# Optimization experiments

Measured on AMD Instinct MI355X. Metric: run time of the kernel, lower is better.

Reference implementation:

```python
import jax, jax.numpy as jnp
import numpy as np

NUM_EXPERTS = 8
NUM_ROWS = 8192
HIDDEN = 2048
INTER = 2048
TOPK = 2


def setup_inputs() -> dict:
    key = jax.random.key(0)
    ks = jax.random.split(key, 5)
    x = jax.random.normal(ks[0], (NUM_ROWS, HIDDEN), dtype=jnp.float32)
    router_probs = jax.random.uniform(ks[1], (NUM_ROWS, NUM_EXPERTS), dtype=jnp.float32)
    # parameters ~ U(-0.1, 0.1) as in nn.init.uniform_
    fc1 = jax.random.uniform(ks[2], (NUM_EXPERTS, HIDDEN, INTER), minval=-0.1, maxval=0.1, dtype=jnp.float32)
    fc2 = jax.random.uniform(ks[3], (NUM_EXPERTS, INTER, HIDDEN), minval=-0.1, maxval=0.1, dtype=jnp.float32)
    fc3 = jax.random.uniform(ks[4], (NUM_EXPERTS, HIDDEN, INTER), minval=-0.1, maxval=0.1, dtype=jnp.float32)
    return {"x": x, "router_probs": router_probs, "fc1": fc1, "fc2": fc2, "fc3": fc3}


def reference(x, router_probs, fc1, fc2, fc3):
    # top-k routing + renormalize chosen probs
    topk_probs, topk_idx = jax.lax.top_k(router_probs, TOPK)  # [N, K]
    topk_probs = topk_probs / jnp.sum(topk_probs, axis=1, keepdims=True)
    # combine weight per (token, expert): scatter-add normalized probs
    n = x.shape[0]
    cw = jnp.zeros((n, NUM_EXPERTS), dtype=x.dtype)
    cw = cw.at[jnp.arange(n)[:, None], topk_idx].add(topk_probs)  # [N, E]
    # loop over fixed, small expert set (structurally distinct weights)
    out = jnp.zeros_like(x)
    for e in range(NUM_EXPERTS):
        h1 = x @ fc1[e]                      # [N, inter]
        h3 = x @ fc3[e]                      # [N, inter]
        act = jax.nn.silu(h1) * h3           # SwiGLU
        out = out + cw[:, e:e + 1] * (act @ fc2[e])
    return out
```

## Files before the change

kernel.cpp:

```cpp
#include <hip/hip_runtime.h>
#include <hip/hip_bf16.h>
#include <stdint.h>

#define NEXP 8
#define NROWS 8192
#define HID 2048
#define INTERN 2048
#define CAP 8192
#define KDIM 2048

typedef __attribute__((ext_vector_type(4))) float f32x4;
typedef __attribute__((ext_vector_type(8))) short bf16x8;

__device__ __forceinline__ unsigned short f2bf(float f) {
  union { float f; uint32_t u; } v; v.f = f;
  uint32_t u = v.u;
  uint32_t r = (u + 0x7fffu + ((u >> 16) & 1u)) >> 16;
  return (unsigned short)r;
}
__device__ __forceinline__ float bf2f(unsigned short u) {
  union { uint32_t u; float f; } v; v.u = (uint32_t)u << 16; return v.f;
}
__device__ __forceinline__ void gload16(const unsigned short* g, char* l) {
  __builtin_amdgcn_global_load_lds((const __attribute__((address_space(1))) void*)g,
                                   (__attribute__((address_space(3))) void*)l,
                                   16, 0, 0);
}

__global__ __launch_bounds__(256) void xcast_kernel(const float* __restrict__ x,
                                                    unsigned short* __restrict__ xb) {
  size_t i = ((size_t)blockIdx.x * 256 + threadIdx.x) * 8;
  size_t stride = (size_t)gridDim.x * 256 * 8;
  const size_t tot = (size_t)NROWS * HID;
  for (; i < tot; i += stride) {
    float4 a = *reinterpret_cast<const float4*>(x + i);
    float4 b = *reinterpret_cast<const float4*>(x + i + 4);
    unsigned short u[8];
    u[0] = f2bf(a.x); u[1] = f2bf(a.y); u[2] = f2bf(a.z); u[3] = f2bf(a.w);
    u[4] = f2bf(b.x); u[5] = f2bf(b.y); u[6] = f2bf(b.z); u[7] = f2bf(b.w);
    *reinterpret_cast<int4*>(xb + i) = *reinterpret_cast<const int4*>(u);
  }
}

__global__ void router_kernel(const float* __restrict__ probs,
                              int* __restrict__ cnt,
                              int* __restrict__ brow,
                              float* __restrict__ bw) {
  int row = blockIdx.x * blockDim.x + threadIdx.x;
  if (row >= NROWS) return;
  float p[8];
#pragma unroll
  for (int j = 0; j < 8; j++) p[j] = probs[row * 8 + j];
  int i1 = 0; float v1 = p[0];
#pragma unroll
  for (int j = 1; j < 8; j++) if (p[j] > v1) { v1 = p[j]; i1 = j; }
  int i2 = -1; float v2 = -1e30f;
#pragma unroll
  for (int j = 0; j < 8; j++) if (j != i1 && p[j] > v2) { v2 = p[j]; i2 = j; }
  float s = v1 + v2;
  float w1 = v1 / s, w2 = v2 / s;
  int pos1 = atomicAdd(&cnt[i1], 1);
  brow[i1 * CAP + pos1] = row; bw[i1 * CAP + pos1] = w1;
  int pos2 = atomicAdd(&cnt[i2], 1);
  brow[i2 * CAP + pos2] = row; bw[i2 * CAP + pos2] = w2;
}

__global__ void offsets_kernel(const int* __restrict__ cnt, int* __restrict__ ofs) {
  if (threadIdx.x == 0 && blockIdx.x == 0) {
    int a = 0;
    for (int e = 0; e < NEXP; e++) { ofs[e] = a; a += cnt[e]; }
  }
}

__global__ __launch_bounds__(256) void transpose_cast_kernel(const float* __restrict__ src,
                                                             unsigned short* __restrict__ dst) {
  __shared__ float tile[64][65];
  const int e = blockIdx.z;
  const int k0 = blockIdx.y * 64;
  const int n0 = blockIdx.x * 64;
  const float* s = src + (size_t)e * KDIM * KDIM;
  unsigned short* d = dst + (size_t)e * KDIM * KDIM;
  const int t = threadIdx.x;
  const int rr = t >> 4, cc = (t & 15) * 4;
#pragma unroll
  for (int i = 0; i < 4; i++) {
    float4 v = *reinterpret_cast<const float4*>(s + (size_t)(k0 + rr + i * 16) * KDIM + n0 + cc);
    tile[rr + i * 16][cc + 0] = v.x; tile[rr + i * 16][cc + 1] = v.y;
    tile[rr + i * 16][cc + 2] = v.z; tile[rr + i * 16][cc + 3] = v.w;
  }
  __syncthreads();
  const int n = t >> 2, kk0 = (t & 3) * 16;
  unsigned short u[16];
#pragma unroll
  for (int j = 0; j < 16; j++) u[j] = f2bf(tile[kk0 + j][n]);
  *reinterpret_cast<int4*>(d + (size_t)(n0 + n) * KDIM + k0 + kk0 + 0) = *reinterpret_cast<const int4*>(&u[0]);
  *reinterpret_cast<int4*>(d + (size_t)(n0 + n) * KDIM + k0 + kk0 + 8) = *reinterpret_cast<const int4*>(&u[8]);
}

template <int EPI>
__global__ __launch_bounds__(256, 2)
void gemm_kernel(const unsigned short* __restrict__ A,
                 const unsigned short* __restrict__ W,
                 const int* __restrict__ cnt, const int* __restrict__ ofs,
                 const int* __restrict__ brow, const float* __restrict__ bw,
                 unsigned short* __restrict__ hbuf,
                 float* __restrict__ out) {
  const int e = blockIdx.z, mt = blockIdx.y, nt = blockIdx.x;
  const int Me = cnt[e];
  if (mt * 128 >= Me) return;
  __shared__ unsigned short As[128 * 64];
  __shared__ unsigned short Bs[128 * 64];
  __shared__ int ridx[128];
  __shared__ float rww[128];
  const int t = threadIdx.x, lane = t & 63, wave = t >> 6;
  const int oe = ofs[e];
  if (t < 128) {
    int sl = mt * 128 + t;
    int ok = sl < Me;
    ridx[t] = ok ? brow[e * CAP + sl] : 0;
    rww[t] = ok ? bw[e * CAP + sl] : 0.f;
  }
  __syncthreads();

  const int srow = t >> 3;
  const int jslot = t & 7;
  const int kg = (jslot ^ (srow & 7)) * 8;
  const unsigned short *pA0, *pA1, *pA2, *pA3;
  if (EPI == 2) {
    int s;
    s = mt * 128 + srow +  0; if (s >= Me) s = 0; pA0 = A + (size_t)(oe + s) * KDIM + kg;
    s = mt * 128 + srow + 32; if (s >= Me) s = 0; pA1 = A + (size_t)(oe + s) * KDIM + kg;
    s = mt * 128 + srow + 64; if (s >= Me) s = 0; pA2 = A + (size_t)(oe + s) * KDIM + kg;
    s = mt * 128 + srow + 96; if (s >= Me) s = 0; pA3 = A + (size_t)(oe + s) * KDIM + kg;
  } else {
    pA0 = A + (size_t)ridx[srow +  0] * KDIM + kg;
    pA1 = A + (size_t)ridx[srow + 32] * KDIM + kg;
    pA2 = A + (size_t)ridx[srow + 64] * KDIM + kg;
    pA3 = A + (size_t)ridx[srow + 96] * KDIM + kg;
  }
  const unsigned short* Wb = W + (size_t)e * KDIM * KDIM;
  const unsigned short* pB0 = Wb + (size_t)(nt * 128 + srow +  0) * KDIM + kg;
  const unsigned short* pB1 = Wb + (size_t)(nt * 128 + srow + 32) * KDIM + kg;
  const unsigned short* pB2 = Wb + (size_t)(nt * 128 + srow + 64) * KDIM + kg;
  const unsigned short* pB3 = Wb + (size_t)(nt * 128 + srow + 96) * KDIM + kg;
  char* dA = (char*)As + wave * 1024;
  char* dB = (char*)Bs + wave * 1024;

  const int wm = wave >> 1, wn = wave & 1;
  const int l15 = lane & 15, kq = lane >> 4;
  const int c0 = (kq * 16) ^ ((l15 & 7) << 4);
  const int aoff = (wm * 64 + l15) * 128;
  const int boff = (wn * 64 + l15) * 128;

  f32x4 acc[4][4] = {};

  for (int k0 = 0; k0 < KDIM; k0 += 64) {
    gload16(pA0, dA);         gload16(pA1, dA + 4096);
    gload16(pA2, dA + 8192);  gload16(pA3, dA + 12288);
    gload16(pB0, dB);         gload16(pB1, dB + 4096);
    gload16(pB2, dB + 8192);  gload16(pB3, dB + 12288);
    pA0 += 64; pA1 += 64; pA2 += 64; pA3 += 64;
    pB0 += 64; pB1 += 64; pB2 += 64; pB3 += 64;
    __syncthreads();

    bf16x8 af0[4], bf0[4], af1[4], bf1[4];
#pragma unroll
    for (int i = 0; i < 4; i++) {
      af0[i] = *reinterpret_cast<const bf16x8*>((const char*)As + aoff + i * 2048 + c0);
      bf0[i] = *reinterpret_cast<const bf16x8*>((const char*)Bs + boff + i * 2048 + c0);
    }
#pragma unroll
    for (int mi = 0; mi < 4; mi++)
#pragma unroll
      for (int ni = 0; ni < 4; ni++)
        acc[mi][ni] = __builtin_amdgcn_mfma_f32_16x16x32_bf16(af0[mi], bf0[ni], acc[mi][ni], 0, 0, 0);
#pragma unroll
    for (int i = 0; i < 4; i++) {
      af1[i] = *reinterpret_cast<const bf16x8*>((const char*)As + aoff + i * 2048 + (c0 ^ 64));
      bf1[i] = *reinterpret_cast<const bf16x8*>((const char*)Bs + boff + i * 2048 + (c0 ^ 64));
    }
#pragma unroll
    for (int mi = 0; mi < 4; mi++)
#pragma unroll
      for (int ni = 0; ni < 4; ni++)
        acc[mi][ni] = __builtin_amdgcn_mfma_f32_16x16x32_bf16(af1[mi], bf1[ni], acc[mi][ni], 0, 0, 0);
    __syncthreads();
  }

  const int slot0 = oe + mt * 128;
#pragma unroll
  for (int mi = 0; mi < 4; mi++) {
#pragma unroll
    for (int ni = 0; ni < 4; ni++) {
      const int coln = nt * 128 + wn * 64 + ni * 16 + l15;
#pragma unroll
      for (int r = 0; r < 4; r++) {
        const int lrow = wm * 64 + mi * 16 + kq * 4 + r;
        if (mt * 128 + lrow < Me) {
          if (EPI == 0) {
            hbuf[(size_t)(slot0 + lrow) * KDIM + coln] = f2bf(acc[mi][ni][r]);
          } else if (EPI == 1) {
            size_t idx = (size_t)(slot0 + lrow) * KDIM + coln;
            float h1 = bf2f(hbuf[idx]);
            float sig = 1.f / (1.f + __expf(-h1));
            hbuf[idx] = f2bf(h1 * sig * acc[mi][ni][r]);
          } else {
            float v = acc[mi][ni][r] * rww[lrow];
            unsafeAtomicAdd(&out[(size_t)ridx[lrow] * HID + coln], v);
          }
        }
      }
    }
  }
}

extern "C" void kernel_launch(void* const* d_in, const int* in_sizes, int n_in,
                              void* d_out, int out_size, void* d_ws, size_t ws_size,
                              hipStream_t stream) {
  const float* x     = (const float*)d_in[0];
  const float* probs = (const float*)d_in[1];
  const float* fc1   = (const float*)d_in[2];
  const float* fc2   = (const float*)d_in[3];
  const float* fc3   = (const float*)d_in[4];
  float* out = (float*)d_out;

  char* ws = (char*)d_ws;
  const size_t WSZ = (size_t)NEXP * HID * INTERN * 2;
  unsigned short* wt1 = (unsigned short*)(ws);
  unsigned short* wt3 = (unsigned short*)(ws + WSZ);
  unsigned short* wt2 = (unsigned short*)(ws + 2 * WSZ);
  unsigned short* h1  = (unsigned short*)(ws + 3 * WSZ);
  unsigned short* xb  = (unsigned short*)(ws + 4 * WSZ);
  char* rbase = ws + 4 * WSZ + (size_t)NROWS * HID * 2;
  int*   brow = (int*)  (rbase);
  float* bw   = (float*)(rbase + (size_t)NEXP * CAP * 4);
  int*   cnt  = (int*)  (rbase + 2 * (size_t)NEXP * CAP * 4);
  int*   ofs  = (int*)  (rbase + 2 * (size_t)NEXP * CAP * 4 + 64);

  hipMemsetAsync(d_out, 0, (size_t)out_size * sizeof(float), stream);
  hipMemsetAsync(cnt, 0, 64, stream);

  xcast_kernel<<<2048, 256, 0, stream>>>(x, xb);
  transpose_cast_kernel<<<dim3(32, 32, 8), 256, 0, stream>>>(fc1, wt1);
  transpose_cast_kernel<<<dim3(32, 32, 8), 256, 0, stream>>>(fc3, wt3);
  transpose_cast_kernel<<<dim3(32, 32, 8), 256, 0, stream>>>(fc2, wt2);
  router_kernel<<<NROWS / 256, 256, 0, stream>>>(probs, cnt, brow, bw);
  offsets_kernel<<<1, 64, 0, stream>>>(cnt, ofs);

  gemm_kernel<0><<<dim3(INTERN / 128, CAP / 128, NEXP), 256, 0, stream>>>(xb, wt1, cnt, ofs, brow, bw, h1, out);
  gemm_kernel<1><<<dim3(INTERN / 128, CAP / 128, NEXP), 256, 0, stream>>>(xb, wt3, cnt, ofs, brow, bw, h1, out);
  gemm_kernel<2><<<dim3(HID / 128, CAP / 128, NEXP), 256, 0, stream>>>(h1, wt2, cnt, ofs, brow, bw, h1, out);
}
```

Before: 781.6 us.

## Fuse gate and up projection GEMMs into one dual-accumulator kernel

Merges the fc1 and fc3 expert GEMMs into one kernel that loads each gathered A tile once and computes both products into two accumulator sets, applying SiLU*up in the epilogue. This removes one pass over the gathered activations, the intermediate bf16 write and reread of h1, and one kernel launch. In exchange, register pressure doubles (two 4x4 f32x4 accumulators) under launch_bounds(256,2) and LDS use grows by a third tile, which may spill or cut occupancy. It also drops a rounding step, since h1 is no longer stored as bf16 before the activation.

```diff
diff --git a/kernel.cpp b/kernel.cpp
--- a/kernel.cpp
+++ b/kernel.cpp
@@ -97,14 +97,112 @@
   *reinterpret_cast<int4*>(d + (size_t)(n0 + n) * KDIM + k0 + kk0 + 8) = *reinterpret_cast<const int4*>(&u[8]);
 }
 
-template <int EPI>
 __global__ __launch_bounds__(256, 2)
-void gemm_kernel(const unsigned short* __restrict__ A,
-                 const unsigned short* __restrict__ W,
-                 const int* __restrict__ cnt, const int* __restrict__ ofs,
-                 const int* __restrict__ brow, const float* __restrict__ bw,
-                 unsigned short* __restrict__ hbuf,
-                 float* __restrict__ out) {
+void gemm13_kernel(const unsigned short* __restrict__ A,
+                   const unsigned short* __restrict__ W1,
+                   const unsigned short* __restrict__ W3,
+                   const int* __restrict__ cnt, const int* __restrict__ ofs,
+                   const int* __restrict__ brow,
+                   unsigned short* __restrict__ act) {
+  const int e = blockIdx.z, mt = blockIdx.y, nt = blockIdx.x;
+  const int Me = cnt[e];
+  if (mt * 128 >= Me) return;
+  __shared__ unsigned short As[128 * 64];
+  __shared__ unsigned short B1s[128 * 64];
+  __shared__ unsigned short B3s[128 * 64];
+  __shared__ int ridx[128];
+  const int t = threadIdx.x, lane = t & 63, wave = t >> 6;
+  const int oe = ofs[e];
+  if (t < 128) {
+    int sl = mt * 128 + t;
+    ridx[t] = (sl < Me) ? brow[e * CAP + sl] : 0;
+  }
+  __syncthreads();
+
+  const int srow = t >> 3;
+  const int kg = ((t & 7) ^ (srow & 7)) * 8;
+  const unsigned short* pA0 = A + (size_t)ridx[srow +  0] * KDIM + kg;
+  const unsigned short* pA1 = A + (size_t)ridx[srow + 32] * KDIM + kg;
+  const unsigned short* pA2 = A + (size_t)ridx[srow + 64] * KDIM + kg;
+  const unsigned short* pA3 = A + (size_t)ridx[srow + 96] * KDIM + kg;
+  const unsigned short* pB0 = W1 + (size_t)e * KDIM * KDIM + (size_t)(nt * 128 + srow) * KDIM + kg;
+  const ptrdiff_t dW = W3 - W1;
+  char* dA  = (char*)As  + wave * 1024;
+  char* dB1 = (char*)B1s + wave * 1024;
+  char* dB3 = (char*)B3s + wave * 1024;
+
+  const int wm = wave >> 1, wn = wave & 1;
+  const int l15 = lane & 15, kq = lane >> 4;
+  const int c0 = (kq * 16) ^ ((l15 & 7) << 4);
+  const int aoff = (wm * 64 + l15) * 128;
+  const int boff = (wn * 64 + l15) * 128;
+
+  f32x4 acc1[4][4] = {};
+  f32x4 acc3[4][4] = {};
+
+  for (int k0 = 0; k0 < KDIM; k0 += 64) {
+    gload16(pA0, dA);                    gload16(pA1, dA + 4096);
+    gload16(pA2, dA + 8192);             gload16(pA3, dA + 12288);
+    gload16(pB0,                dB1);    gload16(pB0 +  32 * KDIM, dB1 + 4096);
+    gload16(pB0 + 64 * KDIM,    dB1 + 8192); gload16(pB0 + 96 * KDIM, dB1 + 12288);
+    gload16(pB0 + dW,           dB3);    gload16(pB0 + dW + 32 * KDIM, dB3 + 4096);
+    gload16(pB0 + dW + 64 * KDIM, dB3 + 8192); gload16(pB0 + dW + 96 * KDIM, dB3 + 12288);
+    pA0 += 64; pA1 += 64; pA2 += 64; pA3 += 64; pB0 += 64;
+    __syncthreads();
+
+#pragma unroll
+    for (int h = 0; h < 2; h++) {
+      const int ch = h ? (c0 ^ 64) : c0;
+      bf16x8 af[4], bf[4];
+#pragma unroll
+      for (int i = 0; i < 4; i++)
+        af[i] = *reinterpret_cast<const bf16x8*>((const char*)As + aoff + i * 2048 + ch);
+#pragma unroll
+      for (int i = 0; i < 4; i++)
+        bf[i] = *reinterpret_cast<const bf16x8*>((const char*)B1s + boff + i * 2048 + ch);
+#pragma unroll
+      for (int mi = 0; mi < 4; mi++)
+#pragma unroll
+        for (int ni = 0; ni < 4; ni++)
+          acc1[mi][ni] = __builtin_amdgcn_mfma_f32_16x16x32_bf16(af[mi], bf[ni], acc1[mi][ni], 0, 0, 0);
+#pragma unroll
+      for (int i = 0; i < 4; i++)
+        bf[i] = *reinterpret_cast<const bf16x8*>((const char*)B3s + boff + i * 2048 + ch);
+#pragma unroll
+      for (int mi = 0; mi < 4; mi++)
+#pragma unroll
+        for (int ni = 0; ni < 4; ni++)
+          acc3[mi][ni] = __builtin_amdgcn_mfma_f32_16x16x32_bf16(af[mi], bf[ni], acc3[mi][ni], 0, 0, 0);
+    }
+    __syncthreads();
+  }
+
+  const int slot0 = oe + mt * 128;
+#pragma unroll
+  for (int mi = 0; mi < 4; mi++) {
+#pragma unroll
+    for (int ni = 0; ni < 4; ni++) {
+      const int coln = nt * 128 + wn * 64 + ni * 16 + l15;
+#pragma unroll
+      for (int r = 0; r < 4; r++) {
+        const int lrow = wm * 64 + mi * 16 + kq * 4 + r;
+        if (mt * 128 + lrow < Me) {
+          float h1 = acc1[mi][ni][r];
+          float h3 = acc3[mi][ni][r];
+          float sig = 1.f / (1.f + __expf(-h1));
+          act[(size_t)(slot0 + lrow) * KDIM + coln] = f2bf(h1 * sig * h3);
+        }
+      }
+    }
+  }
+}
+
+__global__ __launch_bounds__(256, 2)
+void gemm2_kernel(const unsigned short* __restrict__ A,
+                  const unsigned short* __restrict__ W,
+                  const int* __restrict__ cnt, const int* __restrict__ ofs,
+                  const int* __restrict__ brow, const float* __restrict__ bw,
+                  float* __restrict__ out) {
   const int e = blockIdx.z, mt = blockIdx.y, nt = blockIdx.x;
   const int Me = cnt[e];
   if (mt * 128 >= Me) return;
@@ -123,26 +221,14 @@
   __syncthreads();
 
   const int srow = t >> 3;
-  const int jslot = t & 7;
-  const int kg = (jslot ^ (srow & 7)) * 8;
+  const int kg = ((t & 7) ^ (srow & 7)) * 8;
+  int s;
   const unsigned short *pA0, *pA1, *pA2, *pA3;
-  if (EPI == 2) {
-    int s;
-    s = mt * 128 + srow +  0; if (s >= Me) s = 0; pA0 = A + (size_t)(oe + s) * KDIM + kg;
-    s = mt * 128 + srow + 32; if (s >= Me) s = 0; pA1 = A + (size_t)(oe + s) * KDIM + kg;
-    s = mt * 128 + srow + 64; if (s >= Me) s = 0; pA2 = A + (size_t)(oe + s) * KDIM + kg;
-    s = mt * 128 + srow + 96; if (s >= Me) s = 0; pA3 = A + (size_t)(oe + s) * KDIM + kg;
-  } else {
-    pA0 = A + (size_t)ridx[srow +  0] * KDIM + kg;
-    pA1 = A + (size_t)ridx[srow + 32] * KDIM + kg;
-    pA2 = A + (size_t)ridx[srow + 64] * KDIM + kg;
-    pA3 = A + (size_t)ridx[srow + 96] * KDIM + kg;
-  }
-  const unsigned short* Wb = W + (size_t)e * KDIM * KDIM;
-  const unsigned short* pB0 = Wb + (size_t)(nt * 128 + srow +  0) * KDIM + kg;
-  const unsigned short* pB1 = Wb + (size_t)(nt * 128 + srow + 32) * KDIM + kg;
-  const unsigned short* pB2 = Wb + (size_t)(nt * 128 + srow + 64) * KDIM + kg;
-  const unsigned short* pB3 = Wb + (size_t)(nt * 128 + srow + 96) * KDIM + kg;
+  s = mt * 128 + srow +  0; if (s >= Me) s = 0; pA0 = A + (size_t)(oe + s) * KDIM + kg;
+  s = mt * 128 + srow + 32; if (s >= Me) s = 0; pA1 = A + (size_t)(oe + s) * KDIM + kg;
+  s = mt * 128 + srow + 64; if (s >= Me) s = 0; pA2 = A + (size_t)(oe + s) * KDIM + kg;
+  s = mt * 128 + srow + 96; if (s >= Me) s = 0; pA3 = A + (size_t)(oe + s) * KDIM + kg;
+  const unsigned short* pB0 = W + (size_t)e * KDIM * KDIM + (size_t)(nt * 128 + srow) * KDIM + kg;
   char* dA = (char*)As + wave * 1024;
   char* dB = (char*)Bs + wave * 1024;
 
@@ -157,37 +243,29 @@
   for (int k0 = 0; k0 < KDIM; k0 += 64) {
     gload16(pA0, dA);         gload16(pA1, dA + 4096);
     gload16(pA2, dA + 8192);  gload16(pA3, dA + 12288);
-    gload16(pB0, dB);         gload16(pB1, dB + 4096);
-    gload16(pB2, dB + 8192);  gload16(pB3, dB + 12288);
-    pA0 += 64; pA1 += 64; pA2 += 64; pA3 += 64;
-    pB0 += 64; pB1 += 64; pB2 += 64; pB3 += 64;
+    gload16(pB0,             dB);        gload16(pB0 + 32 * KDIM, dB + 4096);
+    gload16(pB0 + 64 * KDIM, dB + 8192); gload16(pB0 + 96 * KDIM, dB + 12288);
+    pA0 += 64; pA1 += 64; pA2 += 64; pA3 += 64; pB0 += 64;
     __syncthreads();
 
-    bf16x8 af0[4], bf0[4], af1[4], bf1[4];
-#pragma unroll
-    for (int i = 0; i < 4; i++) {
-      af0[i] = *reinterpret_cast<const bf16x8*>((const char*)As + aoff + i * 2048 + c0);
-      bf0[i] = *reinterpret_cast<const bf16x8*>((const char*)Bs + boff + i * 2048 + c0);
+#pragma unroll
+    for (int h = 0; h < 2; h++) {
+      const int ch = h ? (c0 ^ 64) : c0;
+      bf16x8 af[4], bf[4];
+#pragma unroll
+      for (int i = 0; i < 4; i++) {
+        af[i] = *reinterpret_cast<const bf16x8*>((const char*)As + aoff + i * 2048 + ch);
+        bf[i] = *reinterpret_cast<const bf16x8*>((const char*)Bs + boff + i * 2048 + ch);
+      }
+#pragma unroll
+      for (int mi = 0; mi < 4; mi++)
+#pragma unroll
+        for (int ni = 0; ni < 4; ni++)
+          acc[mi][ni] = __builtin_amdgcn_mfma_f32_16x16x32_bf16(af[mi], bf[ni], acc[mi][ni], 0, 0, 0);
     }
-#pragma unroll
-    for (int mi = 0; mi < 4; mi++)
-#pragma unroll
-      for (int ni = 0; ni < 4; ni++)
-        acc[mi][ni] = __builtin_amdgcn_mfma_f32_16x16x32_bf16(af0[mi], bf0[ni], acc[mi][ni], 0, 0, 0);
-#pragma unroll
-    for (int i = 0; i < 4; i++) {
-      af1[i] = *reinterpret_cast<const bf16x8*>((const char*)As + aoff + i * 2048 + (c0 ^ 64));
-      bf1[i] = *reinterpret_cast<const bf16x8*>((const char*)Bs + boff + i * 2048 + (c0 ^ 64));
-    }
-#pragma unroll
-    for (int mi = 0; mi < 4; mi++)
-#pragma unroll
-      for (int ni = 0; ni < 4; ni++)
-        acc[mi][ni] = __builtin_amdgcn_mfma_f32_16x16x32_bf16(af1[mi], bf1[ni], acc[mi][ni], 0, 0, 0);
     __syncthreads();
   }
 
-  const int slot0 = oe + mt * 128;
 #pragma unroll
   for (int mi = 0; mi < 4; mi++) {
 #pragma unroll
@@ -197,17 +275,8 @@
       for (int r = 0; r < 4; r++) {
         const int lrow = wm * 64 + mi * 16 + kq * 4 + r;
         if (mt * 128 + lrow < Me) {
-          if (EPI == 0) {
-            hbuf[(size_t)(slot0 + lrow) * KDIM + coln] = f2bf(acc[mi][ni][r]);
-          } else if (EPI == 1) {
-            size_t idx = (size_t)(slot0 + lrow) * KDIM + coln;
-            float h1 = bf2f(hbuf[idx]);
-            float sig = 1.f / (1.f + __expf(-h1));
-            hbuf[idx] = f2bf(h1 * sig * acc[mi][ni][r]);
-          } else {
-            float v = acc[mi][ni][r] * rww[lrow];
-            unsafeAtomicAdd(&out[(size_t)ridx[lrow] * HID + coln], v);
-          }
+          float v = acc[mi][ni][r] * rww[lrow];
+          unsafeAtomicAdd(&out[(size_t)ridx[lrow] * HID + coln], v);
         }
       }
     }
@@ -229,7 +298,7 @@
   unsigned short* wt1 = (unsigned short*)(ws);
   unsigned short* wt3 = (unsigned short*)(ws + WSZ);
   unsigned short* wt2 = (unsigned short*)(ws + 2 * WSZ);
-  unsigned short* h1  = (unsigned short*)(ws + 3 * WSZ);
+  unsigned short* act = (unsigned short*)(ws + 3 * WSZ);
   unsigned short* xb  = (unsigned short*)(ws + 4 * WSZ);
   char* rbase = ws + 4 * WSZ + (size_t)NROWS * HID * 2;
   int*   brow = (int*)  (rbase);
@@ -247,7 +316,6 @@
   router_kernel<<<NROWS / 256, 256, 0, stream>>>(probs, cnt, brow, bw);
   offsets_kernel<<<1, 64, 0, stream>>>(cnt, ofs);
 
-  gemm_kernel<0><<<dim3(INTERN / 128, CAP / 128, NEXP), 256, 0, stream>>>(xb, wt1, cnt, ofs, brow, bw, h1, out);
-  gemm_kernel<1><<<dim3(INTERN / 128, CAP / 128, NEXP), 256, 0, stream>>>(xb, wt3, cnt, ofs, brow, bw, h1, out);
-  gemm_kernel<2><<<dim3(HID / 128, CAP / 128, NEXP), 256, 0, stream>>>(h1, wt2, cnt, ofs, brow, bw, h1, out);
-}
+  gemm13_kernel<<<dim3(INTERN / 128, CAP / 128, NEXP), 256, 0, stream>>>(xb, wt1, wt3, cnt, ofs, brow, act);
+  gemm2_kernel<<<dim3(HID / 128, CAP / 128, NEXP), 256, 0, stream>>>(act, wt2, cnt, ofs, brow, bw, out);
+}
```

New measurement: 731.3 us. 6.4% less time.
